# Kernel optimization log

Measured on AMD Instinct MI355X. Metric: run time of the kernel, lower is better.

Reference implementation:

```python
import jax, jax.numpy as jnp
import numpy as np

GRID = 5
ELEMS = GRID * GRID  # 25 values per puzzle grid


def _dup_count(rows):
    """rows: [B, 5, 5]; counts, per row, elements equal to an earlier element
    in the same row (i.e. 5 - num_unique per row, summed). Returns scalar."""
    # eq[b, i, j, k] = rows[b, i, j] == rows[b, i, k]
    eq = rows[:, :, :, None] == rows[:, :, None, :]
    # strictly-lower mask over (j, k): only k < j counts as 'seen earlier'
    earlier = jnp.tril(jnp.ones((GRID, GRID), dtype=bool), k=-1)
    dup = jnp.any(eq & earlier, axis=-1)  # [B, 5, 5]
    return jnp.sum(dup.astype(jnp.float32))


def setup_inputs() -> dict:
    key = jax.random.key(0)
    k1, k2 = jax.random.split(key)
    n = 26214400  # 1,048,576 grids * 25
    preds = jax.random.normal(k1, (n,), dtype=jnp.float32)
    targets = jax.random.randint(k2, (n,), 0, 6, dtype=jnp.int32)
    return {"preds": preds, "targets": targets}


def reference(preds, targets):
    preds_flat = preds.reshape(-1)
    # loss1: mean absolute error against float-cast integer targets
    loss1 = jnp.mean(jnp.abs(preds_flat - targets.astype(jnp.float32)))

    batch_size = targets.shape[0] // ELEMS
    # duplicate counting runs on detached predictions (original uses .detach().cpu().numpy())
    grids = jax.lax.stop_gradient(preds_flat).reshape(batch_size, GRID, GRID)
    total_dup = _dup_count(grids) + _dup_count(jnp.swapaxes(grids, 1, 2))
    loss2 = total_dup / batch_size * 0.1

    # out-of-bounds penalty: .any().item() has no gradient path
    p = jax.lax.stop_gradient(preds_flat)
    oob = jnp.any((p < 0.5) | (p > 5.5))
    return loss1 + loss2 + jnp.where(oob, jnp.float32(1000.0), jnp.float32(0.0))
```

## Files before the change

kernel.cpp:

```cpp
#include <hip/hip_runtime.h>


#define BLOCK 256
#define WPB 4
#define TILE 1600
#define NBLOCKS 768

typedef float v4f __attribute__((ext_vector_type(4)));
typedef int   v4i __attribute__((ext_vector_type(4)));

struct TileRegs {
    v4f p[6];
    v4i t[6];
    float ptl;
    int   ttl;
};

__device__ __forceinline__ void load_tile(const float* __restrict__ preds,
                                          const int* __restrict__ tgts,
                                          long long t, int lane, TileRegs& r) {
    const v4f* __restrict__ p4 = (const v4f*)(preds + t * TILE);
    const v4i* __restrict__ t4 = (const v4i*)(tgts  + t * TILE);
    #pragma unroll
    for (int k = 0; k < 6; ++k) r.p[k] = __builtin_nontemporal_load(&p4[lane + 64 * k]);
    #pragma unroll
    for (int k = 0; k < 6; ++k) r.t[k] = __builtin_nontemporal_load(&t4[lane + 64 * k]);
    r.ptl = __builtin_nontemporal_load(&preds[t * TILE + 1536 + lane]);
    r.ttl = __builtin_nontemporal_load(&tgts [t * TILE + 1536 + lane]);
}

__device__ __forceinline__ int grid_dups(const float* __restrict__ p) {
    int ldup = 0;
    #pragma unroll
    for (int r = 0; r < 5; ++r) {
        const float a = p[r*5+0], b = p[r*5+1], c = p[r*5+2],
                    d = p[r*5+3], e = p[r*5+4];
        ldup += (int)(b == a);
        ldup += (int)((c == a) | (c == b));
        ldup += (int)((d == a) | (d == b) | (d == c));
        ldup += (int)((e == a) | (e == b) | (e == c) | (e == d));
    }
    #pragma unroll
    for (int q = 0; q < 5; ++q) {
        const float a = p[q+0], b = p[q+5], c = p[q+10],
                    d = p[q+15], e = p[q+20];
        ldup += (int)(b == a);
        ldup += (int)((c == a) | (c == b));
        ldup += (int)((d == a) | (d == b) | (d == c));
        ldup += (int)((e == a) | (e == b) | (e == c) | (e == d));
    }
    return ldup;
}

__device__ __forceinline__ void compute_tile(const TileRegs& r,
                                             float* __restrict__ wp,
                                             v4f* __restrict__ wp4,
                                             int lane, float& lsum, int& ldup,
                                             float& mn, float& mx) {
    #pragma unroll
    for (int k = 0; k < 6; ++k) {
        wp4[lane + 64 * k] = r.p[k];
        lsum += fabsf(r.p[k].x - (float)r.t[k].x);
        lsum += fabsf(r.p[k].y - (float)r.t[k].y);
        lsum += fabsf(r.p[k].z - (float)r.t[k].z);
        lsum += fabsf(r.p[k].w - (float)r.t[k].w);
        mn = fminf(mn, fminf(fminf(r.p[k].x, r.p[k].y), fminf(r.p[k].z, r.p[k].w)));
        mx = fmaxf(mx, fmaxf(fmaxf(r.p[k].x, r.p[k].y), fmaxf(r.p[k].z, r.p[k].w)));
    }
    wp[1536 + lane] = r.ptl;
    lsum += fabsf(r.ptl - (float)r.ttl);
    mn = fminf(mn, r.ptl);
    mx = fmaxf(mx, r.ptl);

    ldup += grid_dups(wp + lane * 25);
}

__global__ __launch_bounds__(BLOCK, 1) void puzzle_main(
    const float* __restrict__ preds, const int* __restrict__ tgts,
    long long n_total,
    float* __restrict__ blk_sum, int* __restrict__ blk_dup,
    int* __restrict__ blk_oob)
{
    __shared__ float lds_p[WPB * TILE];
    __shared__ float s_sum[WPB];
    __shared__ int   s_dup[WPB];
    __shared__ int   s_oob[WPB];

    const int tid  = threadIdx.x;
    const int lane = tid & 63;
    const int wv   = tid >> 6;

    const long long total_tiles = n_total / TILE;
    const int total_waves = gridDim.x * WPB;
    const int gwave = blockIdx.x * WPB + wv;

    float* __restrict__ wp = &lds_p[wv * TILE];
    v4f* __restrict__ wp4 = reinterpret_cast<v4f*>(wp);

    float lsum = 0.0f;
    int   ldup = 0;
    float mn =  1e30f;
    float mx = -1e30f;

    long long t0 = gwave;
    if (t0 < total_tiles) {
        TileRegs cur, nxt;
        load_tile(preds, tgts, t0, lane, cur);
        __builtin_amdgcn_sched_barrier(0);
        for (long long tn = t0 + total_waves; tn < total_tiles; tn += total_waves) {
            load_tile(preds, tgts, tn, lane, nxt);
            __builtin_amdgcn_sched_barrier(0);
            compute_tile(cur, wp, wp4, lane, lsum, ldup, mn, mx);
            cur = nxt;
        }
        compute_tile(cur, wp, wp4, lane, lsum, ldup, mn, mx);
    }

    const long long rem = n_total - total_tiles * TILE;
    if (rem > 0 && gwave == total_waves - 1) {
        const int ngrids = (int)(rem / 25);
        if (lane < ngrids) {
            const float* sp = preds + total_tiles * TILE + (long long)lane * 25;
            const int*   st = tgts  + total_tiles * TILE + (long long)lane * 25;
            float q[25];
            #pragma unroll
            for (int j = 0; j < 25; ++j) q[j] = sp[j];
            #pragma unroll
            for (int j = 0; j < 25; ++j) {
                lsum += fabsf(q[j] - (float)st[j]);
                mn = fminf(mn, q[j]);
                mx = fmaxf(mx, q[j]);
            }
            ldup += grid_dups(q);
        }
    }

    #pragma unroll
    for (int off = 32; off > 0; off >>= 1) {
        lsum += __shfl_down(lsum, off, 64);
        ldup += __shfl_down(ldup, off, 64);
        mn = fminf(mn, __shfl_down(mn, off, 64));
        mx = fmaxf(mx, __shfl_down(mx, off, 64));
    }
    if (lane == 0) {
        s_sum[wv] = lsum;
        s_dup[wv] = ldup;
        s_oob[wv] = (int)((mn < 0.5f) | (mx > 5.5f));
    }
    __syncthreads();
    if (tid == 0) {
        float bs = 0.0f; int bd = 0, bo = 0;
        #pragma unroll
        for (int w = 0; w < WPB; ++w) { bs += s_sum[w]; bd += s_dup[w]; bo |= s_oob[w]; }
        blk_sum[blockIdx.x] = bs;
        blk_dup[blockIdx.x] = bd;
        blk_oob[blockIdx.x] = bo;
    }
}

#define FBLOCK 256
#define FNWAVES (FBLOCK / 64)

__global__ __launch_bounds__(FBLOCK) void puzzle_final(
    const float* __restrict__ blk_sum, const int* __restrict__ blk_dup,
    const int* __restrict__ blk_oob, int nblocks,
    long long n_total, long long batch, float* __restrict__ out)
{
    __shared__ double s_sum[FNWAVES];
    __shared__ int    s_dup[FNWAVES];
    __shared__ int    s_oob[FNWAVES];

    double lsum = 0.0;
    int ldup = 0, loob = 0;
    for (int i = threadIdx.x; i < nblocks; i += FBLOCK) {
        lsum += (double)blk_sum[i];
        ldup += blk_dup[i];
        loob |= blk_oob[i];
    }
    #pragma unroll
    for (int off = 32; off > 0; off >>= 1) {
        lsum += __shfl_down(lsum, off, 64);
        ldup += __shfl_down(ldup, off, 64);
        loob |= __shfl_down(loob, off, 64);
    }
    const int wave = threadIdx.x >> 6;
    if ((threadIdx.x & 63) == 0) { s_sum[wave] = lsum; s_dup[wave] = ldup; s_oob[wave] = loob; }
    __syncthreads();
    if (threadIdx.x == 0) {
        double bs = 0.0; int bd = 0, bo = 0;
        #pragma unroll
        for (int w = 0; w < FNWAVES; ++w) { bs += s_sum[w]; bd += s_dup[w]; bo |= s_oob[w]; }
        const float loss1 = (float)(bs / (double)n_total);
        const float loss2 = (float)((double)bd * 0.1 / (double)batch);
        out[0] = loss1 + loss2 + (bo ? 1000.0f : 0.0f);
    }
}

extern "C" void kernel_launch(void* const* d_in, const int* in_sizes, int n_in,
                              void* d_out, int out_size, void* d_ws, size_t ws_size,
                              hipStream_t stream) {
    const float* preds = (const float*)d_in[0];
    const int*   tgts  = (const int*)d_in[1];
    float* out = (float*)d_out;

    const long long n = (long long)in_sizes[0];
    const long long batch = n / 25;

    float* blk_sum = (float*)d_ws;
    int*   blk_dup = (int*)(blk_sum + NBLOCKS);
    int*   blk_oob = (int*)(blk_dup + NBLOCKS);

    puzzle_main<<<NBLOCKS, BLOCK, 0, stream>>>(preds, tgts, n,
                                               blk_sum, blk_dup, blk_oob);
    puzzle_final<<<1, FBLOCK, 0, stream>>>(blk_sum, blk_dup, blk_oob,
                                           NBLOCKS, n, batch, out);
}
```

Measured before the change: 202.6 us.

## Fuse final reduction via last-block ticket and ping-pong tile loop

Replaces the separate single-block finalize kernel with an atomic ticket counter so the last main-kernel block performs the cross-block reduction and writes the output. The prefetch loop is also restructured into an A/B ping-pong that avoids copying the next-tile registers into the current ones each iteration. This removes one kernel launch and the register move, but adds a memset on the stream and an atomic plus fences per block.

```diff
diff --git a/kernel.cpp b/kernel.cpp
--- a/kernel.cpp
+++ b/kernel.cpp
@@ -77,14 +77,19 @@
 
 __global__ __launch_bounds__(BLOCK, 1) void puzzle_main(
     const float* __restrict__ preds, const int* __restrict__ tgts,
-    long long n_total,
+    long long n_total, long long batch,
     float* __restrict__ blk_sum, int* __restrict__ blk_dup,
-    int* __restrict__ blk_oob)
+    int* __restrict__ blk_oob,
+    unsigned* __restrict__ ticket, float* __restrict__ out)
 {
     __shared__ float lds_p[WPB * TILE];
     __shared__ float s_sum[WPB];
     __shared__ int   s_dup[WPB];
     __shared__ int   s_oob[WPB];
+    __shared__ int   s_last;
+    __shared__ double f_sum[WPB];
+    __shared__ int    f_dup[WPB];
+    __shared__ int    f_oob[WPB];
 
     const int tid  = threadIdx.x;
     const int lane = tid & 63;
@@ -102,18 +107,33 @@
     float mn =  1e30f;
     float mx = -1e30f;
 
-    long long t0 = gwave;
-    if (t0 < total_tiles) {
-        TileRegs cur, nxt;
-        load_tile(preds, tgts, t0, lane, cur);
+    const long long stride = total_waves;
+    long long tA = gwave;
+    if (tA < total_tiles) {
+        TileRegs A, B;
+        long long tB = tA + stride;
+        load_tile(preds, tgts, tA, lane, A);
         __builtin_amdgcn_sched_barrier(0);
-        for (long long tn = t0 + total_waves; tn < total_tiles; tn += total_waves) {
-            load_tile(preds, tgts, tn, lane, nxt);
+        if (tB < total_tiles) {
+            load_tile(preds, tgts, tB, lane, B);
             __builtin_amdgcn_sched_barrier(0);
-            compute_tile(cur, wp, wp4, lane, lsum, ldup, mn, mx);
-            cur = nxt;
-        }
-        compute_tile(cur, wp, wp4, lane, lsum, ldup, mn, mx);
+        }
+        for (;;) {
+            compute_tile(A, wp, wp4, lane, lsum, ldup, mn, mx);
+            tA += 2 * stride;
+            if (tA < total_tiles) {
+                load_tile(preds, tgts, tA, lane, A);
+                __builtin_amdgcn_sched_barrier(0);
+            }
+            if (tB >= total_tiles) break;
+            compute_tile(B, wp, wp4, lane, lsum, ldup, mn, mx);
+            tB += 2 * stride;
+            if (tB < total_tiles) {
+                load_tile(preds, tgts, tB, lane, B);
+                __builtin_amdgcn_sched_barrier(0);
+            }
+            if (tA >= total_tiles) break;
+        }
     }
 
     const long long rem = n_total - total_tiles * TILE;
@@ -155,44 +175,42 @@
         blk_sum[blockIdx.x] = bs;
         blk_dup[blockIdx.x] = bd;
         blk_oob[blockIdx.x] = bo;
-    }
-}
-
-#define FBLOCK 256
-#define FNWAVES (FBLOCK / 64)
-
-__global__ __launch_bounds__(FBLOCK) void puzzle_final(
-    const float* __restrict__ blk_sum, const int* __restrict__ blk_dup,
-    const int* __restrict__ blk_oob, int nblocks,
-    long long n_total, long long batch, float* __restrict__ out)
-{
-    __shared__ double s_sum[FNWAVES];
-    __shared__ int    s_dup[FNWAVES];
-    __shared__ int    s_oob[FNWAVES];
-
-    double lsum = 0.0;
-    int ldup = 0, loob = 0;
-    for (int i = threadIdx.x; i < nblocks; i += FBLOCK) {
-        lsum += (double)blk_sum[i];
-        ldup += blk_dup[i];
-        loob |= blk_oob[i];
-    }
-    #pragma unroll
-    for (int off = 32; off > 0; off >>= 1) {
-        lsum += __shfl_down(lsum, off, 64);
-        ldup += __shfl_down(ldup, off, 64);
-        loob |= __shfl_down(loob, off, 64);
-    }
-    const int wave = threadIdx.x >> 6;
-    if ((threadIdx.x & 63) == 0) { s_sum[wave] = lsum; s_dup[wave] = ldup; s_oob[wave] = loob; }
+        __threadfence();
+        const unsigned old = __hip_atomic_fetch_add(ticket, 1u, __ATOMIC_ACQ_REL,
+                                                    __HIP_MEMORY_SCOPE_AGENT);
+        s_last = (old == (unsigned)(gridDim.x - 1));
+    }
     __syncthreads();
-    if (threadIdx.x == 0) {
-        double bs = 0.0; int bd = 0, bo = 0;
+
+    if (s_last) {
+        __threadfence();
+        const int nblocks = (int)gridDim.x;
+        double fsum = 0.0;
+        int fdup = 0, foob = 0;
+        for (int i = tid; i < nblocks; i += BLOCK) {
+            fsum += (double)__hip_atomic_load(&blk_sum[i], __ATOMIC_RELAXED,
+                                              __HIP_MEMORY_SCOPE_AGENT);
+            fdup += __hip_atomic_load(&blk_dup[i], __ATOMIC_RELAXED,
+                                      __HIP_MEMORY_SCOPE_AGENT);
+            foob |= __hip_atomic_load(&blk_oob[i], __ATOMIC_RELAXED,
+                                      __HIP_MEMORY_SCOPE_AGENT);
+        }
         #pragma unroll
-        for (int w = 0; w < FNWAVES; ++w) { bs += s_sum[w]; bd += s_dup[w]; bo |= s_oob[w]; }
-        const float loss1 = (float)(bs / (double)n_total);
-        const float loss2 = (float)((double)bd * 0.1 / (double)batch);
-        out[0] = loss1 + loss2 + (bo ? 1000.0f : 0.0f);
+        for (int off = 32; off > 0; off >>= 1) {
+            fsum += __shfl_down(fsum, off, 64);
+            fdup += __shfl_down(fdup, off, 64);
+            foob |= __shfl_down(foob, off, 64);
+        }
+        if (lane == 0) { f_sum[wv] = fsum; f_dup[wv] = fdup; f_oob[wv] = foob; }
+        __syncthreads();
+        if (tid == 0) {
+            double bs = 0.0; int bd = 0, bo = 0;
+            #pragma unroll
+            for (int w = 0; w < WPB; ++w) { bs += f_sum[w]; bd += f_dup[w]; bo |= f_oob[w]; }
+            const float loss1 = (float)(bs / (double)n_total);
+            const float loss2 = (float)((double)bd * 0.1 / (double)batch);
+            out[0] = loss1 + loss2 + (bo ? 1000.0f : 0.0f);
+        }
     }
 }
 
@@ -206,12 +224,14 @@
     const long long n = (long long)in_sizes[0];
     const long long batch = n / 25;
 
-    float* blk_sum = (float*)d_ws;
-    int*   blk_dup = (int*)(blk_sum + NBLOCKS);
-    int*   blk_oob = (int*)(blk_dup + NBLOCKS);
-
-    puzzle_main<<<NBLOCKS, BLOCK, 0, stream>>>(preds, tgts, n,
-                                               blk_sum, blk_dup, blk_oob);
-    puzzle_final<<<1, FBLOCK, 0, stream>>>(blk_sum, blk_dup, blk_oob,
-                                           NBLOCKS, n, batch, out);
-}
+    unsigned* ticket = (unsigned*)d_ws;
+    float* blk_sum = (float*)((char*)d_ws + 16);
+    int*   blk_dup = (int*)((char*)d_ws + 16 + 4 * NBLOCKS);
+    int*   blk_oob = (int*)((char*)d_ws + 16 + 8 * NBLOCKS);
+
+    hipMemsetAsync(ticket, 0, sizeof(unsigned), stream);
+
+    puzzle_main<<<NBLOCKS, BLOCK, 0, stream>>>(preds, tgts, n, batch,
+                                               blk_sum, blk_dup, blk_oob,
+                                               ticket, out);
+}
```

After: 257.1 us. +26.9%, slower.
